# Performance work log

Hardware: AMD Instinct MI355X
Metric: run time of the kernel (lower is better)

Reference implementation:

```python
import jax, jax.numpy as jnp
import numpy as np

N_NODES = 300000
DIM = 64
NNZ = 4800000


def setup_inputs() -> dict:
    key = jax.random.key(0)
    ks = jax.random.split(key, 8)
    emb_all = 0.1 * jax.random.normal(ks[0], (N_NODES, DIM), dtype=jnp.float32)
    # edge values ~ symmetric-normalized adjacency scale (avg degree 16 -> ~1/16)
    vals = jax.random.uniform(ks[1], (NNZ,), dtype=jnp.float32) * (1.0 / 16.0)
    vals2 = jax.random.uniform(ks[2], (NNZ,), dtype=jnp.float32) * (1.0 / 16.0)
    rows = jnp.sort(jax.random.randint(ks[3], (NNZ,), 0, N_NODES, dtype=jnp.int32))
    cols = jax.random.randint(ks[4], (NNZ,), 0, N_NODES, dtype=jnp.int32)
    rows2 = jnp.sort(jax.random.randint(ks[5], (NNZ,), 0, N_NODES, dtype=jnp.int32))
    cols2 = jax.random.randint(ks[6], (NNZ,), 0, N_NODES, dtype=jnp.int32)
    return {
        "emb_all": emb_all,
        "vals": vals,
        "vals2": vals2,
        "rows": rows,
        "cols": cols,
        "rows2": rows2,
        "cols2": cols2,
        "n_layers": 3,
        "num_users": 100000,
    }


def _spmm(rows, cols, vals, x, n):
    # sparse [n,n] @ dense [n,d] via gather + segment-sum
    return jax.ops.segment_sum(vals[:, None] * x[cols], rows, num_segments=n)


def _pearson(x, y):
    # per-row pearson correlation over the last (latent) dim -> [N]
    xd = x - jnp.mean(x, axis=-1, keepdims=True)
    yd = y - jnp.mean(y, axis=-1, keepdims=True)
    num = jnp.sum(xd * yd, axis=-1)
    den = jnp.sqrt(jnp.sum(xd * xd, axis=-1)) * jnp.sqrt(jnp.sum(yd * yd, axis=-1))
    den = jnp.where(den < 1e-7, jnp.float32(1e-7), den)
    return num / den


def reference(emb_all, vals, vals2, rows, cols, rows2, cols2, n_layers, num_users):
    n = emb_all.shape[0]
    e0 = emb_all
    embs2 = [e0]
    # layer 0: plain LightGCN propagation on G
    e = _spmm(rows, cols, vals, e0, n)
    embs2.append(e)
    # layers 1..n_layers: pearson-gated propagation on G2
    for _ in range(n_layers):
        b = _pearson(embs2[-1], e0)  # [N]
        prop = _spmm(rows2, cols2, vals2, embs2[-1], n)
        e = b[:, None] * prop + (1.0 - b)[:, None] * e0
        embs2.append(e)
    light_out = jnp.mean(jnp.stack(embs2, axis=1), axis=1)  # [N, d]
    users = light_out[:num_users]
    items = light_out[num_users:]
    return users, items
```

## Files before the change

kernel.cpp:

```cpp
#include <hip/hip_runtime.h>

#define DIM 64
#define SC  32.0f
#define ISC 0.03125f

typedef __attribute__((ext_vector_type(4))) float f4;
typedef __attribute__((ext_vector_type(2))) float f2;
typedef __attribute__((ext_vector_type(4))) unsigned int u4;
typedef __attribute__((ext_vector_type(2))) unsigned int u2;

#define ONE2 0x3f803f80u

__device__ __forceinline__ float bflo(unsigned u) { return __uint_as_float(u << 16); }
__device__ __forceinline__ float bfhi(unsigned u) { return __uint_as_float(u & 0xffff0000u); }
__device__ __forceinline__ unsigned bfr(float f) {
    unsigned u = __float_as_uint(f);
    return (u + 0x7fffu + ((u >> 16) & 1u)) >> 16;
}
__device__ __forceinline__ unsigned packbf(float e, float o) { return bfr(e) | (bfr(o) << 16); }
__device__ __forceinline__ unsigned cvtpk(float lo, float hi) {
    unsigned r;
    asm("v_cvt_pk_bf16_f32 %0, %1, %2" : "=v"(r) : "v"(lo), "v"(hi));
    return r;
}
__device__ __forceinline__ float dot2bf(unsigned a, unsigned b, float c) {
    float d;
    asm("v_dot2_f32_bf16 %0, %1, %2, %3" : "=v"(d) : "v"(a), "v"(b), "v"(c));
    return d;
}
__device__ __forceinline__ float gsum8(float v) {
    v += __shfl_xor(v, 1, 64);
    v += __shfl_xor(v, 2, 64);
    v += __shfl_xor(v, 4, 64);
    return v;
}

__global__ void build_row_ptr2_kernel(const int* __restrict__ rowsA, int nnzA,
                                      const int* __restrict__ rowsB, int nnzB,
                                      int n, int* __restrict__ rpA,
                                      int* __restrict__ rpB) {
    int i = blockIdx.x * blockDim.x + threadIdx.x;
    const int* rows; int nnz; int* rp; int r;
    if (i <= n) { rows = rowsA; nnz = nnzA; rp = rpA; r = i; }
    else {
        r = i - (n + 1);
        if (r > n) return;
        rows = rowsB; nnz = nnzB; rp = rpB;
    }
    int lo = 0, hi = nnz;
    while (lo < hi) {
        int mid = (lo + hi) >> 1;
        if (rows[mid] < r) lo = mid + 1; else hi = mid;
    }
    rp[r] = lo;
}

__global__ void cvt_kernel(const float* __restrict__ in,
                           unsigned int* __restrict__ obf,
                           unsigned char* __restrict__ of8, int n8) {
    int i = blockIdx.x * blockDim.x + threadIdx.x;
    if (i >= n8) return;
    const f4* p = (const f4*)in + 2 * (size_t)i;
    f4 a = p[0], b = p[1];
    u4 o;
    o.x = packbf(a.x, a.y); o.y = packbf(a.z, a.w);
    o.z = packbf(b.x, b.y); o.w = packbf(b.z, b.w);
    ((u4*)obf)[i] = o;
    int lo = 0, hi = 0;
    lo = __builtin_amdgcn_cvt_pk_fp8_f32(a.x * SC, a.y * SC, lo, false);
    lo = __builtin_amdgcn_cvt_pk_fp8_f32(a.z * SC, a.w * SC, lo, true);
    hi = __builtin_amdgcn_cvt_pk_fp8_f32(b.x * SC, b.y * SC, hi, false);
    hi = __builtin_amdgcn_cvt_pk_fp8_f32(b.z * SC, b.w * SC, hi, true);
    u2 w8; w8.x = (unsigned)lo; w8.y = (unsigned)hi;
    ((u2*)of8)[i] = w8;
}

template <int MODE, bool SUM>
__global__ __launch_bounds__(256) void layer_kernel(
    const unsigned short* __restrict__ t0,
    const unsigned char*  __restrict__ gtab,
    const float* __restrict__ vals, const int* __restrict__ cols,
    const int* __restrict__ rp, int n,
    unsigned short* __restrict__ bfout,
    unsigned char*  __restrict__ f8out,
    const unsigned short* __restrict__ e1in,
    const unsigned short* __restrict__ e3in,
    const unsigned short* __restrict__ s12in,
    f2* __restrict__ stats, float* __restrict__ bbuf,
    float* __restrict__ out)
{
    const int tid  = threadIdx.x;
    const int lane = tid & 63;
    const int j    = lane & 7;
    const int wave = blockIdx.x * (blockDim.x >> 6) + (tid >> 6);
    const int rowg = wave * 8 + (lane >> 3);
    const bool valid = rowg < n;
    const int rg   = valid ? rowg : n - 1;

    const int start = rp[rg];
    const int end   = rp[rg + 1];
    const int len   = valid ? (end - start) : 0;
    const int b0    = start & ~1;
    const int doff  = b0 - start;

    int ml = len;
    ml = max(ml, __shfl_xor(ml, 8, 64));
    ml = max(ml, __shfl_xor(ml, 16, 64));
    ml = max(ml, __shfl_xor(ml, 32, 64));
    const int steps = (ml + 8) >> 3;

    const unsigned joff8 = (unsigned)(j << 3);
    const size_t ro = (size_t)rg << 6;

    float bcoef = 0.f;
    if (MODE != 0) bcoef = __builtin_nontemporal_load(bbuf + rg);
    u4 yr = __builtin_nontemporal_load((const u4*)(t0 + ro) + j);
    f2 st = {};
    if (MODE == 1) st = __builtin_nontemporal_load(stats + rg);

    f2 a01 = {0.f, 0.f}, a23 = {0.f, 0.f}, a45 = {0.f, 0.f}, a67 = {0.f, 0.f};

    for (int s = 0; s < steps; ++s) {
        const int k = b0 + (s << 3);
        u2 c01 = __builtin_nontemporal_load((const u2*)(cols + k));
        u2 c23 = __builtin_nontemporal_load((const u2*)(cols + k + 2));
        u2 c45 = __builtin_nontemporal_load((const u2*)(cols + k + 4));
        u2 c67 = __builtin_nontemporal_load((const u2*)(cols + k + 6));
        f2 v01 = __builtin_nontemporal_load((const f2*)(vals + k));
        f2 v23 = __builtin_nontemporal_load((const f2*)(vals + k + 2));
        f2 v45 = __builtin_nontemporal_load((const f2*)(vals + k + 4));
        f2 v67 = __builtin_nontemporal_load((const f2*)(vals + k + 6));
        const int rel = (s << 3) + doff;
        bool ok0 = (unsigned)(rel)     < (unsigned)len;
        bool ok1 = (unsigned)(rel + 1) < (unsigned)len;
        bool ok2 = (unsigned)(rel + 2) < (unsigned)len;
        bool ok3 = (unsigned)(rel + 3) < (unsigned)len;
        bool ok4 = (unsigned)(rel + 4) < (unsigned)len;
        bool ok5 = (unsigned)(rel + 5) < (unsigned)len;
        bool ok6 = (unsigned)(rel + 6) < (unsigned)len;
        bool ok7 = (unsigned)(rel + 7) < (unsigned)len;
        unsigned cc0 = ok0 ? (unsigned)c01.x : 0u;
        unsigned cc1 = ok1 ? (unsigned)c01.y : 0u;
        unsigned cc2 = ok2 ? (unsigned)c23.x : 0u;
        unsigned cc3 = ok3 ? (unsigned)c23.y : 0u;
        unsigned cc4 = ok4 ? (unsigned)c45.x : 0u;
        unsigned cc5 = ok5 ? (unsigned)c45.y : 0u;
        unsigned cc6 = ok6 ? (unsigned)c67.x : 0u;
        unsigned cc7 = ok7 ? (unsigned)c67.y : 0u;
        u2 g0 = *(const u2*)(gtab + ((cc0 << 6) + joff8));
        u2 g1 = *(const u2*)(gtab + ((cc1 << 6) + joff8));
        u2 g2 = *(const u2*)(gtab + ((cc2 << 6) + joff8));
        u2 g3 = *(const u2*)(gtab + ((cc3 << 6) + joff8));
        u2 g4 = *(const u2*)(gtab + ((cc4 << 6) + joff8));
        u2 g5 = *(const u2*)(gtab + ((cc5 << 6) + joff8));
        u2 g6 = *(const u2*)(gtab + ((cc6 << 6) + joff8));
        u2 g7 = *(const u2*)(gtab + ((cc7 << 6) + joff8));
        float w0 = ok0 ? v01.x : 0.f;
        float w1 = ok1 ? v01.y : 0.f;
        float w2 = ok2 ? v23.x : 0.f;
        float w3 = ok3 ? v23.y : 0.f;
        float w4 = ok4 ? v45.x : 0.f;
        float w5 = ok5 ? v45.y : 0.f;
        float w6 = ok6 ? v67.x : 0.f;
        float w7 = ok7 ? v67.y : 0.f;
#define CONS(gg, ww) {                                                        \
        f2 wv; wv.x = (ww); wv.y = (ww);                                      \
        f2 p0 = __builtin_amdgcn_cvt_pk_f32_fp8((int)gg.x, false);            \
        f2 p1 = __builtin_amdgcn_cvt_pk_f32_fp8((int)gg.x, true);             \
        f2 p2 = __builtin_amdgcn_cvt_pk_f32_fp8((int)gg.y, false);            \
        f2 p3 = __builtin_amdgcn_cvt_pk_f32_fp8((int)gg.y, true);             \
        a01 += wv * p0; a23 += wv * p1; a45 += wv * p2; a67 += wv * p3;       \
    }
        CONS(g0, w0) CONS(g1, w1) CONS(g2, w2) CONS(g3, w3)
        CONS(g4, w4) CONS(g5, w5) CONS(g6, w6) CONS(g7, w7)
#undef CONS
    }

    float acc[8] = { a01.x * ISC, a01.y * ISC, a23.x * ISC, a23.y * ISC,
                     a45.x * ISC, a45.y * ISC, a67.x * ISC, a67.y * ISC };

    if (MODE == 0) {
        float sy  = dot2bf(yr.x, ONE2,
                    dot2bf(yr.y, ONE2, dot2bf(yr.z, ONE2, dot2bf(yr.w, ONE2, 0.f))));
        float syy = dot2bf(yr.x, yr.x,
                    dot2bf(yr.y, yr.y, dot2bf(yr.z, yr.z, dot2bf(yr.w, yr.w, 0.f))));
        sy = gsum8(sy); syy = gsum8(syy);
        float my  = sy * (1.f / 64.f);
        float vy  = syy - sy * my;
        float svy = sqrtf(fmaxf(vy, 0.f));
        u4 o;
        o.x = cvtpk(acc[0], acc[1]); o.y = cvtpk(acc[2], acc[3]);
        o.z = cvtpk(acc[4], acc[5]); o.w = cvtpk(acc[6], acc[7]);
        float sx  = dot2bf(o.x, ONE2,
                    dot2bf(o.y, ONE2, dot2bf(o.z, ONE2, dot2bf(o.w, ONE2, 0.f))));
        float sxx = dot2bf(o.x, o.x,
                    dot2bf(o.y, o.y, dot2bf(o.z, o.z, dot2bf(o.w, o.w, 0.f))));
        float sxy = dot2bf(o.x, yr.x,
                    dot2bf(o.y, yr.y, dot2bf(o.z, yr.z, dot2bf(o.w, yr.w, 0.f))));
        sx = gsum8(sx); sxx = gsum8(sxx); sxy = gsum8(sxy);
        float mx  = sx * (1.f / 64.f);
        float num = sxy - sx * my;
        float vx  = sxx - sx * mx;
        float den = sqrtf(fmaxf(vx, 0.f)) * svy;
        den = fmaxf(den, 1e-7f);
        float bn = num / den;
        if (valid) {
            if (j == 0) {
                f2 s2; s2.x = my; s2.y = svy;
                __builtin_nontemporal_store(s2, stats + rg);
                __builtin_nontemporal_store(bn, bbuf + rg);
            }
            __builtin_nontemporal_store(o, (u4*)(bfout + ro) + j);
            int lo = 0, hi = 0;
            lo = __builtin_amdgcn_cvt_pk_fp8_f32(acc[0] * SC, acc[1] * SC, lo, false);
            lo = __builtin_amdgcn_cvt_pk_fp8_f32(acc[2] * SC, acc[3] * SC, lo, true);
            hi = __builtin_amdgcn_cvt_pk_fp8_f32(acc[4] * SC, acc[5] * SC, hi, false);
            hi = __builtin_amdgcn_cvt_pk_fp8_f32(acc[6] * SC, acc[7] * SC, hi, true);
            u2 w8; w8.x = (unsigned)lo; w8.y = (unsigned)hi;
            __builtin_nontemporal_store(w8, (u2*)(f8out + (ro  )) + j);
        }
        return;
    }

    const float ob = 1.f - bcoef;
    float y0[8] = { bflo(yr.x), bfhi(yr.x), bflo(yr.y), bfhi(yr.y),
                    bflo(yr.z), bfhi(yr.z), bflo(yr.w), bfhi(yr.w) };
    float en[8];
    #pragma unroll
    for (int i = 0; i < 8; ++i) en[i] = bcoef * acc[i] + ob * y0[i];

    if (MODE == 1) {
        u4 o;
        o.x = cvtpk(en[0], en[1]); o.y = cvtpk(en[2], en[3]);
        o.z = cvtpk(en[4], en[5]); o.w = cvtpk(en[6], en[7]);
        float sx  = dot2bf(o.x, ONE2,
                    dot2bf(o.y, ONE2, dot2bf(o.z, ONE2, dot2bf(o.w, ONE2, 0.f))));
        float sxx = dot2bf(o.x, o.x,
                    dot2bf(o.y, o.y, dot2bf(o.z, o.z, dot2bf(o.w, o.w, 0.f))));
        float sxy = dot2bf(o.x, yr.x,
                    dot2bf(o.y, yr.y, dot2bf(o.z, yr.z, dot2bf(o.w, yr.w, 0.f))));
        sx = gsum8(sx); sxx = gsum8(sxx); sxy = gsum8(sxy);
        float mx  = sx * (1.f / 64.f);
        float num = sxy - sx * st.x;
        float vx  = sxx - sx * mx;
        float den = sqrtf(fmaxf(vx, 0.f)) * st.y;
        den = fmaxf(den, 1e-7f);
        float bn = num / den;
        if (valid) {
            if (j == 0) __builtin_nontemporal_store(bn, bbuf + rg);
            if (SUM) {
                u4 e1r = __builtin_nontemporal_load((const u4*)(e1in + ro) + j);
                u4 so;
                so.x = packbf(bflo(e1r.x) + en[0], bfhi(e1r.x) + en[1]);
                so.y = packbf(bflo(e1r.y) + en[2], bfhi(e1r.y) + en[3]);
                so.z = packbf(bflo(e1r.z) + en[4], bfhi(e1r.z) + en[5]);
                so.w = packbf(bflo(e1r.w) + en[6], bfhi(e1r.w) + en[7]);
                __builtin_nontemporal_store(so, (u4*)(bfout + ro) + j);
            } else {
                __builtin_nontemporal_store(o, (u4*)(bfout + ro) + j);
            }
            int lo = 0, hi = 0;
            lo = __builtin_amdgcn_cvt_pk_fp8_f32(en[0] * SC, en[1] * SC, lo, false);
            lo = __builtin_amdgcn_cvt_pk_fp8_f32(en[2] * SC, en[3] * SC, lo, true);
            hi = __builtin_amdgcn_cvt_pk_fp8_f32(en[4] * SC, en[5] * SC, hi, false);
            hi = __builtin_amdgcn_cvt_pk_fp8_f32(en[6] * SC, en[7] * SC, hi, true);
            u2 w8; w8.x = (unsigned)lo; w8.y = (unsigned)hi;
            __builtin_nontemporal_store(w8, (u2*)(f8out + ro) + j);
        }
    } else {
        u4 xr  = __builtin_nontemporal_load((const u4*)(e3in + ro) + j);
        u4 s12 = __builtin_nontemporal_load((const u4*)(s12in + ro) + j);
        float s[8];
        s[0] = y0[0] + bflo(s12.x) + bflo(xr.x) + en[0];
        s[1] = y0[1] + bfhi(s12.x) + bfhi(xr.x) + en[1];
        s[2] = y0[2] + bflo(s12.y) + bflo(xr.y) + en[2];
        s[3] = y0[3] + bfhi(s12.y) + bfhi(xr.y) + en[3];
        s[4] = y0[4] + bflo(s12.z) + bflo(xr.z) + en[4];
        s[5] = y0[5] + bfhi(s12.z) + bfhi(xr.z) + en[5];
        s[6] = y0[6] + bflo(s12.w) + bflo(xr.w) + en[6];
        s[7] = y0[7] + bfhi(s12.w) + bfhi(xr.w) + en[7];
        if (valid) {
            f4 o0 = { s[0] * 0.2f, s[1] * 0.2f, s[2] * 0.2f, s[3] * 0.2f };
            f4 o1 = { s[4] * 0.2f, s[5] * 0.2f, s[6] * 0.2f, s[7] * 0.2f };
            f4* op = (f4*)(out + ro) + 2 * j;
            __builtin_nontemporal_store(o0, op);
            __builtin_nontemporal_store(o1, op + 1);
        }
    }
}

extern "C" void kernel_launch(void* const* d_in, const int* in_sizes, int n_in,
                              void* d_out, int out_size, void* d_ws, size_t ws_size,
                              hipStream_t stream) {
    const float* emb   = (const float*)d_in[0];
    const float* vals  = (const float*)d_in[1];
    const float* vals2 = (const float*)d_in[2];
    const int*   rows  = (const int*)d_in[3];
    const int*   cols  = (const int*)d_in[4];
    const int*   rows2 = (const int*)d_in[5];
    const int*   cols2 = (const int*)d_in[6];

    const int n    = in_sizes[0] / DIM;
    const int nnz  = in_sizes[1];
    const int nnz2 = in_sizes[2];

    float* out = (float*)d_out;

    char*  ws       = (char*)d_ws;
    size_t rp_bytes = (((size_t)(n + 1) * sizeof(int)) + 255) & ~(size_t)255;
    size_t st_bytes = (((size_t)n * sizeof(f2)) + 255) & ~(size_t)255;
    size_t bb_bytes = (((size_t)n * sizeof(float)) + 255) & ~(size_t)255;
    size_t tb_bytes = (size_t)n * DIM * sizeof(unsigned short);
    size_t f8_bytes = (size_t)n * DIM;
    int*   rp1 = (int*)ws;
    int*   rp2 = (int*)(ws + rp_bytes);
    f2*    ST  = (f2*)(ws + 2 * rp_bytes);
    float* BB  = (float*)(ws + 2 * rp_bytes + st_bytes);
    char*  p   = ws + 2 * rp_bytes + st_bytes + bb_bytes;
    unsigned short* T0  = (unsigned short*)p;              p += tb_bytes;
    unsigned short* E1  = (unsigned short*)p;              p += tb_bytes;
    unsigned short* S12 = (unsigned short*)p;              p += tb_bytes;
    unsigned char*  T0F = (unsigned char*)p;               p += f8_bytes;
    unsigned char*  FA  = (unsigned char*)p;               p += f8_bytes;
    unsigned char*  FB  = (unsigned char*)p;               p += f8_bytes;
    unsigned short* E3  = E1;

    const int tb = 256;
    build_row_ptr2_kernel<<<(2 * (n + 1) + tb - 1) / tb, tb, 0, stream>>>(
        rows, nnz, rows2, nnz2, n, rp1, rp2);

    const int n8 = n * DIM / 8;
    cvt_kernel<<<(n8 + tb - 1) / tb, tb, 0, stream>>>(emb, (unsigned int*)T0, T0F, n8);

    const int waves = (n + 7) / 8;
    const int grid  = (waves + 3) / 4;
    layer_kernel<0, false><<<grid, tb, 0, stream>>>(T0, T0F, vals, cols, rp1, n,
                                                    E1, FA, E1, E1, S12, ST, BB, out);
    layer_kernel<1, true><<<grid, tb, 0, stream>>>(T0, FA, vals2, cols2, rp2, n,
                                                   S12, FB, E1, E1, S12, ST, BB, out);
    layer_kernel<1, false><<<grid, tb, 0, stream>>>(T0, FB, vals2, cols2, rp2, n,
                                                    E3, FA, E1, E1, S12, ST, BB, out);
    layer_kernel<2, false><<<grid, tb, 0, stream>>>(T0, FA, vals2, cols2, rp2, n,
                                                    E3, FA, E1, E3, S12, ST, BB, out);
}
```

Measured before the change: 474.4 us.

## Drop bf16 E1/E3 buffers, reuse fp8 tables for own-row values

Each layer now reads its own row from the fp8 gather table (the previous layer's output) instead of separate bf16 copies. This removes the E1/E3 bf16 writes and reads, and the bf16 T0 read in layer 0. Per-row mean and std statistics of the input embedding move into the conversion kernel, so layer 0 no longer reads T0 in bf16. This cuts per-layer HBM traffic at the cost of fp8 precision for the e1/e3 terms in the Pearson computation and the final mean.

```diff
diff --git a/kernel.cpp b/kernel.cpp
--- a/kernel.cpp
+++ b/kernel.cpp
@@ -57,7 +57,8 @@
 
 __global__ void cvt_kernel(const float* __restrict__ in,
                            unsigned int* __restrict__ obf,
-                           unsigned char* __restrict__ of8, int n8) {
+                           unsigned char* __restrict__ of8,
+                           f2* __restrict__ stats, int n8) {
     int i = blockIdx.x * blockDim.x + threadIdx.x;
     if (i >= n8) return;
     const f4* p = (const f4*)in + 2 * (size_t)i;
@@ -73,6 +74,18 @@
     hi = __builtin_amdgcn_cvt_pk_fp8_f32(b.z * SC, b.w * SC, hi, true);
     u2 w8; w8.x = (unsigned)lo; w8.y = (unsigned)hi;
     ((u2*)of8)[i] = w8;
+    float sy  = dot2bf(o.x, ONE2,
+                dot2bf(o.y, ONE2, dot2bf(o.z, ONE2, dot2bf(o.w, ONE2, 0.f))));
+    float syy = dot2bf(o.x, o.x,
+                dot2bf(o.y, o.y, dot2bf(o.z, o.z, dot2bf(o.w, o.w, 0.f))));
+    sy = gsum8(sy); syy = gsum8(syy);
+    float my  = sy * (1.f / 64.f);
+    float vy  = syy - sy * my;
+    float svy = sqrtf(fmaxf(vy, 0.f));
+    if ((threadIdx.x & 7) == 0) {
+        f2 s2; s2.x = my; s2.y = svy;
+        __builtin_nontemporal_store(s2, stats + (i >> 3));
+    }
 }
 
 template <int MODE, bool SUM>
@@ -83,8 +96,6 @@
     const int* __restrict__ rp, int n,
     unsigned short* __restrict__ bfout,
     unsigned char*  __restrict__ f8out,
-    const unsigned short* __restrict__ e1in,
-    const unsigned short* __restrict__ e3in,
     const unsigned short* __restrict__ s12in,
     f2* __restrict__ stats, float* __restrict__ bbuf,
     float* __restrict__ out)
@@ -114,9 +125,13 @@
 
     float bcoef = 0.f;
     if (MODE != 0) bcoef = __builtin_nontemporal_load(bbuf + rg);
-    u4 yr = __builtin_nontemporal_load((const u4*)(t0 + ro) + j);
+    u4 yr = {};
+    if (MODE != 0) yr = __builtin_nontemporal_load((const u4*)(t0 + ro) + j);
     f2 st = {};
-    if (MODE == 1) st = __builtin_nontemporal_load(stats + rg);
+    if (MODE != 2) st = __builtin_nontemporal_load(stats + rg);
+    u2 gr = {};
+    if (MODE == 0 || SUM || MODE == 2)
+        gr = *(const u2*)(gtab + ro + joff8);
 
     f2 a01 = {0.f, 0.f}, a23 = {0.f, 0.f}, a45 = {0.f, 0.f}, a67 = {0.f, 0.f};
 
@@ -179,45 +194,41 @@
     float acc[8] = { a01.x * ISC, a01.y * ISC, a23.x * ISC, a23.y * ISC,
                      a45.x * ISC, a45.y * ISC, a67.x * ISC, a67.y * ISC };
 
+    f2 q0 = __builtin_amdgcn_cvt_pk_f32_fp8((int)gr.x, false);
+    f2 q1 = __builtin_amdgcn_cvt_pk_f32_fp8((int)gr.x, true);
+    f2 q2 = __builtin_amdgcn_cvt_pk_f32_fp8((int)gr.y, false);
+    f2 q3 = __builtin_amdgcn_cvt_pk_f32_fp8((int)gr.y, true);
+    float grf[8] = { q0.x * ISC, q0.y * ISC, q1.x * ISC, q1.y * ISC,
+                     q2.x * ISC, q2.y * ISC, q3.x * ISC, q3.y * ISC };
+
     if (MODE == 0) {
-        float sy  = dot2bf(yr.x, ONE2,
-                    dot2bf(yr.y, ONE2, dot2bf(yr.z, ONE2, dot2bf(yr.w, ONE2, 0.f))));
-        float syy = dot2bf(yr.x, yr.x,
-                    dot2bf(yr.y, yr.y, dot2bf(yr.z, yr.z, dot2bf(yr.w, yr.w, 0.f))));
-        sy = gsum8(sy); syy = gsum8(syy);
-        float my  = sy * (1.f / 64.f);
-        float vy  = syy - sy * my;
-        float svy = sqrtf(fmaxf(vy, 0.f));
         u4 o;
         o.x = cvtpk(acc[0], acc[1]); o.y = cvtpk(acc[2], acc[3]);
         o.z = cvtpk(acc[4], acc[5]); o.w = cvtpk(acc[6], acc[7]);
+        unsigned yb0 = cvtpk(grf[0], grf[1]), yb1 = cvtpk(grf[2], grf[3]);
+        unsigned yb2 = cvtpk(grf[4], grf[5]), yb3 = cvtpk(grf[6], grf[7]);
         float sx  = dot2bf(o.x, ONE2,
                     dot2bf(o.y, ONE2, dot2bf(o.z, ONE2, dot2bf(o.w, ONE2, 0.f))));
         float sxx = dot2bf(o.x, o.x,
                     dot2bf(o.y, o.y, dot2bf(o.z, o.z, dot2bf(o.w, o.w, 0.f))));
-        float sxy = dot2bf(o.x, yr.x,
-                    dot2bf(o.y, yr.y, dot2bf(o.z, yr.z, dot2bf(o.w, yr.w, 0.f))));
+        float sxy = dot2bf(o.x, yb0,
+                    dot2bf(o.y, yb1, dot2bf(o.z, yb2, dot2bf(o.w, yb3, 0.f))));
         sx = gsum8(sx); sxx = gsum8(sxx); sxy = gsum8(sxy);
         float mx  = sx * (1.f / 64.f);
-        float num = sxy - sx * my;
+        float num = sxy - sx * st.x;
         float vx  = sxx - sx * mx;
-        float den = sqrtf(fmaxf(vx, 0.f)) * svy;
+        float den = sqrtf(fmaxf(vx, 0.f)) * st.y;
         den = fmaxf(den, 1e-7f);
         float bn = num / den;
         if (valid) {
-            if (j == 0) {
-                f2 s2; s2.x = my; s2.y = svy;
-                __builtin_nontemporal_store(s2, stats + rg);
-                __builtin_nontemporal_store(bn, bbuf + rg);
-            }
-            __builtin_nontemporal_store(o, (u4*)(bfout + ro) + j);
+            if (j == 0) __builtin_nontemporal_store(bn, bbuf + rg);
             int lo = 0, hi = 0;
             lo = __builtin_amdgcn_cvt_pk_fp8_f32(acc[0] * SC, acc[1] * SC, lo, false);
             lo = __builtin_amdgcn_cvt_pk_fp8_f32(acc[2] * SC, acc[3] * SC, lo, true);
             hi = __builtin_amdgcn_cvt_pk_fp8_f32(acc[4] * SC, acc[5] * SC, hi, false);
             hi = __builtin_amdgcn_cvt_pk_fp8_f32(acc[6] * SC, acc[7] * SC, hi, true);
             u2 w8; w8.x = (unsigned)lo; w8.y = (unsigned)hi;
-            __builtin_nontemporal_store(w8, (u2*)(f8out + (ro  )) + j);
+            __builtin_nontemporal_store(w8, (u2*)(f8out + ro) + j);
         }
         return;
     }
@@ -249,15 +260,12 @@
         if (valid) {
             if (j == 0) __builtin_nontemporal_store(bn, bbuf + rg);
             if (SUM) {
-                u4 e1r = __builtin_nontemporal_load((const u4*)(e1in + ro) + j);
                 u4 so;
-                so.x = packbf(bflo(e1r.x) + en[0], bfhi(e1r.x) + en[1]);
-                so.y = packbf(bflo(e1r.y) + en[2], bfhi(e1r.y) + en[3]);
-                so.z = packbf(bflo(e1r.z) + en[4], bfhi(e1r.z) + en[5]);
-                so.w = packbf(bflo(e1r.w) + en[6], bfhi(e1r.w) + en[7]);
+                so.x = packbf(grf[0] + en[0], grf[1] + en[1]);
+                so.y = packbf(grf[2] + en[2], grf[3] + en[3]);
+                so.z = packbf(grf[4] + en[4], grf[5] + en[5]);
+                so.w = packbf(grf[6] + en[6], grf[7] + en[7]);
                 __builtin_nontemporal_store(so, (u4*)(bfout + ro) + j);
-            } else {
-                __builtin_nontemporal_store(o, (u4*)(bfout + ro) + j);
             }
             int lo = 0, hi = 0;
             lo = __builtin_amdgcn_cvt_pk_fp8_f32(en[0] * SC, en[1] * SC, lo, false);
@@ -268,17 +276,16 @@
             __builtin_nontemporal_store(w8, (u2*)(f8out + ro) + j);
         }
     } else {
-        u4 xr  = __builtin_nontemporal_load((const u4*)(e3in + ro) + j);
         u4 s12 = __builtin_nontemporal_load((const u4*)(s12in + ro) + j);
         float s[8];
-        s[0] = y0[0] + bflo(s12.x) + bflo(xr.x) + en[0];
-        s[1] = y0[1] + bfhi(s12.x) + bfhi(xr.x) + en[1];
-        s[2] = y0[2] + bflo(s12.y) + bflo(xr.y) + en[2];
-        s[3] = y0[3] + bfhi(s12.y) + bfhi(xr.y) + en[3];
-        s[4] = y0[4] + bflo(s12.z) + bflo(xr.z) + en[4];
-        s[5] = y0[5] + bfhi(s12.z) + bfhi(xr.z) + en[5];
-        s[6] = y0[6] + bflo(s12.w) + bflo(xr.w) + en[6];
-        s[7] = y0[7] + bfhi(s12.w) + bfhi(xr.w) + en[7];
+        s[0] = y0[0] + bflo(s12.x) + grf[0] + en[0];
+        s[1] = y0[1] + bfhi(s12.x) + grf[1] + en[1];
+        s[2] = y0[2] + bflo(s12.y) + grf[2] + en[2];
+        s[3] = y0[3] + bfhi(s12.y) + grf[3] + en[3];
+        s[4] = y0[4] + bflo(s12.z) + grf[4] + en[4];
+        s[5] = y0[5] + bfhi(s12.z) + grf[5] + en[5];
+        s[6] = y0[6] + bflo(s12.w) + grf[6] + en[6];
+        s[7] = y0[7] + bfhi(s12.w) + grf[7] + en[7];
         if (valid) {
             f4 o0 = { s[0] * 0.2f, s[1] * 0.2f, s[2] * 0.2f, s[3] * 0.2f };
             f4 o1 = { s[4] * 0.2f, s[5] * 0.2f, s[6] * 0.2f, s[7] * 0.2f };
@@ -318,28 +325,26 @@
     float* BB  = (float*)(ws + 2 * rp_bytes + st_bytes);
     char*  p   = ws + 2 * rp_bytes + st_bytes + bb_bytes;
     unsigned short* T0  = (unsigned short*)p;              p += tb_bytes;
-    unsigned short* E1  = (unsigned short*)p;              p += tb_bytes;
     unsigned short* S12 = (unsigned short*)p;              p += tb_bytes;
     unsigned char*  T0F = (unsigned char*)p;               p += f8_bytes;
     unsigned char*  FA  = (unsigned char*)p;               p += f8_bytes;
     unsigned char*  FB  = (unsigned char*)p;               p += f8_bytes;
-    unsigned short* E3  = E1;
 
     const int tb = 256;
     build_row_ptr2_kernel<<<(2 * (n + 1) + tb - 1) / tb, tb, 0, stream>>>(
         rows, nnz, rows2, nnz2, n, rp1, rp2);
 
     const int n8 = n * DIM / 8;
-    cvt_kernel<<<(n8 + tb - 1) / tb, tb, 0, stream>>>(emb, (unsigned int*)T0, T0F, n8);
+    cvt_kernel<<<(n8 + tb - 1) / tb, tb, 0, stream>>>(emb, (unsigned int*)T0, T0F, ST, n8);
 
     const int waves = (n + 7) / 8;
     const int grid  = (waves + 3) / 4;
     layer_kernel<0, false><<<grid, tb, 0, stream>>>(T0, T0F, vals, cols, rp1, n,
-                                                    E1, FA, E1, E1, S12, ST, BB, out);
+                                                    S12, FA, S12, ST, BB, out);
     layer_kernel<1, true><<<grid, tb, 0, stream>>>(T0, FA, vals2, cols2, rp2, n,
-                                                   S12, FB, E1, E1, S12, ST, BB, out);
+                                                   S12, FB, S12, ST, BB, out);
     layer_kernel<1, false><<<grid, tb, 0, stream>>>(T0, FB, vals2, cols2, rp2, n,
-                                                    E3, FA, E1, E1, S12, ST, BB, out);
+                                                    S12, FA, S12, ST, BB, out);
     layer_kernel<2, false><<<grid, tb, 0, stream>>>(T0, FA, vals2, cols2, rp2, n,
-                                                    E3, FA, E1, E3, S12, ST, BB, out);
-}
+                                                    S12, FA, S12, ST, BB, out);
+}
```

Result: faster. 456.7 us (-3.7%).
